# Optimization experiments

Hardware: AMD Instinct MI355X
Metric: run time of the kernel (lower is better)

The kernel has to match this reference:

```python
import jax, jax.numpy as jnp
import numpy as np

H_SIZE = 2048
NUM_K_HEADS = 16
NUM_V_HEADS = 32
DK = 128
DV = 128
KEY_DIM = NUM_K_HEADS * DK        # 2048
VALUE_DIM = NUM_V_HEADS * DV      # 4096
CONV_DIM = 2 * KEY_DIM + VALUE_DIM  # 8192
KERNEL = 4
EPS = 1e-6
B, S = 2, 2048


def setup_inputs() -> dict:
    key = jax.random.key(0)
    ks = jax.random.split(key, 8)
    w = lambda k, shape, s: jax.random.normal(k, shape, jnp.float32) * s
    return {
        "hidden_states": jax.random.normal(ks[0], (B, S, H_SIZE), jnp.float32),
        "w_qkv": w(ks[1], (H_SIZE, CONV_DIM), 0.02),
        "w_z": w(ks[2], (H_SIZE, VALUE_DIM), 0.02),
        "w_b": w(ks[3], (H_SIZE, NUM_V_HEADS), 0.02),
        "w_a": w(ks[4], (H_SIZE, NUM_V_HEADS), 0.02),
        "conv_w": w(ks[5], (CONV_DIM, KERNEL), 0.2),
        "dt_bias": jnp.ones((NUM_V_HEADS,), jnp.float32),
        "A_log": jnp.zeros((NUM_V_HEADS,), jnp.float32),
        "norm_gamma": jnp.ones((DV,), jnp.float32),
        "w_out": w(ks[6], (VALUE_DIM, H_SIZE), 0.02),
    }


def _l2norm(x, eps=1e-6):
    return x * jax.lax.rsqrt(jnp.sum(x * x, axis=-1, keepdims=True) + eps)


def _causal_conv(x, w):
    # depthwise causal conv1d; x: (B,S,C), w: (C,K)
    K = w.shape[-1]
    Sq = x.shape[1]
    xp = jnp.pad(x, ((0, 0), (K - 1, 0), (0, 0)))
    out = xp[:, 0:Sq, :] * w[None, None, :, 0]
    for j in range(1, K):  # tiny fixed kernel loop (K=4)
        out = out + xp[:, j:j + Sq, :] * w[None, None, :, j]
    return out


def _forward(hidden_states, w_qkv, w_z, w_b, w_a, conv_w, dt_bias, A_log,
             norm_gamma, w_out):
    Bq, Sq, _ = hidden_states.shape
    mixed = hidden_states @ w_qkv                       # (B,S,CONV_DIM)
    z = (hidden_states @ w_z).reshape(Bq, Sq, NUM_V_HEADS, DV)
    b = hidden_states @ w_b                             # (B,S,Hv)
    a = hidden_states @ w_a                             # (B,S,Hv)
    mixed = jax.nn.silu(_causal_conv(mixed, conv_w))
    q, k, v = jnp.split(mixed, [KEY_DIM, 2 * KEY_DIM], axis=-1)
    q = q.reshape(Bq, Sq, NUM_K_HEADS, DK)
    k = k.reshape(Bq, Sq, NUM_K_HEADS, DK)
    v = v.reshape(Bq, Sq, NUM_V_HEADS, DV)
    nrep = NUM_V_HEADS // NUM_K_HEADS
    q = jnp.repeat(q, nrep, axis=2)                     # GQA expand -> Hv heads
    k = jnp.repeat(k, nrep, axis=2)
    beta = jax.nn.sigmoid(b)                            # write gate
    g = -jnp.exp(A_log)[None, None, :] * jax.nn.softplus(a + dt_bias[None, None, :])

    # gated delta rule recurrence in float32 (matches reference)
    qf = _l2norm(q.astype(jnp.float32)) * (DK ** -0.5)
    kf = _l2norm(k.astype(jnp.float32))
    vf = v.astype(jnp.float32)
    gf = g.astype(jnp.float32)
    bf = beta.astype(jnp.float32)

    def step(state, xs):
        q_t, k_t, v_t, g_t, b_t = xs  # (B,H,dk),(B,H,dk),(B,H,dv),(B,H),(B,H)
        state = state * jnp.exp(g_t)[..., None, None]
        kv = jnp.einsum('bhk,bhkv->bhv', k_t, state)
        delta = (v_t - kv) * b_t[..., None]
        state = state + jnp.einsum('bhk,bhv->bhkv', k_t, delta)
        out = jnp.einsum('bhk,bhkv->bhv', q_t, state)
        return state, out

    mv = lambda x: jnp.moveaxis(x, 1, 0)  # (B,S,...) -> (S,B,...)
    xs = (mv(qf), mv(kf), mv(vf), mv(gf), mv(bf))
    state0 = jnp.zeros((Bq, NUM_V_HEADS, DK, DV), jnp.float32)
    _, outs = jax.lax.scan(step, state0, xs)            # (S,B,H,dv)
    o = jnp.moveaxis(outs, 0, 1)                        # (B,S,H,dv)

    # gated RMSNorm over head_v_dim: gate with silu(z), then rms-normalize
    o = o * jax.nn.silu(z.astype(jnp.float32))
    o = o * jax.lax.rsqrt(jnp.mean(o * o, axis=-1, keepdims=True) + EPS)
    o = o * norm_gamma
    o = o.reshape(Bq, Sq, VALUE_DIM).astype(hidden_states.dtype)
    return o @ w_out


def reference(hidden_states, w_qkv, w_z, w_b, w_a, conv_w, dt_bias, A_log,
              norm_gamma, w_out):
    return _forward(hidden_states, w_qkv, w_z, w_b, w_a, conv_w, dt_bias,
                    A_log, norm_gamma, w_out)
```

## Files before the change

### kernel.cpp

```cpp
#include <hip/hip_runtime.h>
#include <hip/hip_bf16.h>
#include <cstdint>


#define HSZ 2048
#define NUM_K_HEADS 16
#define NUM_V_HEADS 32
#define DKH 128
#define DVH 128
#define KEY_DIM 2048
#define VALUE_DIM 4096
#define CONV_DIM 8192
#define BB 2
#define SSEQ 2048
#define MM (BB * SSEQ)
#define CHUNK 64
#define NCHUNK (SSEQ / CHUNK)
#define DVB 16

typedef __hip_bfloat16 bf16;
typedef short short8 __attribute__((ext_vector_type(8)));
typedef float f32x4 __attribute__((ext_vector_type(4)));

__device__ __forceinline__ float bfu(ushort u) {
  union { float f; uint32_t i; } x;
  x.i = ((uint32_t)u) << 16;
  return x.f;
}
__device__ __forceinline__ ushort f2b(float f) {
  bf16 h = __float2bfloat16(f);
  return *reinterpret_cast<ushort*>(&h);
}

__device__ __forceinline__ void gload16(const void* g, const void* l) {
  __builtin_amdgcn_global_load_lds(
      (const __attribute__((address_space(1))) unsigned int*)g,
      (__attribute__((address_space(3))) unsigned int*)(const_cast<void*>(l)),
      16, 0, 0);
}

__device__ __forceinline__ int kidx(int r, int d) {
  return r * 128 + (((d >> 3) ^ (r & 7)) << 3) + (d & 7);
}
__device__ __forceinline__ int widx(int r, int d) {
  return r * 64 + (((d >> 3) ^ (r & 7)) << 3) + (d & 7);
}

__global__ __launch_bounds__(256) void cast_bf16_kernel(
    const float* __restrict__ in, ushort* __restrict__ out, int n4) {
  int i = blockIdx.x * 256 + threadIdx.x;
  if (i < n4) {
    float4 v = ((const float4*)in)[i];
    ushort4 u;
    u.x = f2b(v.x); u.y = f2b(v.y); u.z = f2b(v.z); u.w = f2b(v.w);
    ((ushort4*)out)[i] = u;
  }
}

__global__ __launch_bounds__(256) void transpose_cast(
    const float* __restrict__ W, ushort* __restrict__ WT, int K, int N) {
  __shared__ ushort tile[32][33];
  const int tx = threadIdx.x & 31, ty = threadIdx.x >> 5;
  const int n0 = blockIdx.x * 32, k0 = blockIdx.y * 32;
#pragma unroll
  for (int i = 0; i < 4; ++i)
    tile[ty + i * 8][tx] = f2b(W[(size_t)(k0 + ty + i * 8) * N + n0 + tx]);
  __syncthreads();
#pragma unroll
  for (int i = 0; i < 4; ++i)
    WT[(size_t)(n0 + ty + i * 8) * K + k0 + tx] = tile[tx][ty + i * 8];
}

__global__ __launch_bounds__(512) void gemm256(
    const ushort* __restrict__ A, const ushort* __restrict__ BT,
    ushort* __restrict__ Cv, int M, int N, int K) {
  __shared__ __align__(16) ushort smem[256 * 264];
  const int t = threadIdx.x;
  const int w = t >> 6, lane = t & 63;
  const int m0 = blockIdx.y * 256, n0 = blockIdx.x * 256;
  const int wm = (w >> 2) * 128, wn = (w & 3) * 64;
  const int fr = lane & 15, kb = lane >> 4;
  const int srow = t >> 3;
  const int scol = (t & 7) * 8;
  const int ssw = ((scol >> 3) ^ (srow & 7)) << 3;
  const int rsw = fr & 7;
  f32x4 acc[8][4] = {};
  const int nt = K / 64;

#define STAGE_TILE(tt, buf)                                                   \
  {                                                                           \
    const int k0_ = (tt)*64;                                                  \
    ushort* As_ = smem + (buf)*32768;                                         \
    ushort* Bs_ = As_ + 16384;                                                \
    _Pragma("unroll") for (int p = 0; p < 4; ++p) {                           \
      const int row_ = p * 64 + srow;                                         \
      gload16(&A[(size_t)(m0 + row_) * K + k0_ + ssw],                        \
              &As_[row_ * 64 + scol]);                                        \
    }                                                                         \
    _Pragma("unroll") for (int p = 0; p < 4; ++p) {                           \
      const int row_ = p * 64 + srow;                                         \
      gload16(&BT[(size_t)(n0 + row_) * K + k0_ + ssw],                       \
              &Bs_[row_ * 64 + scol]);                                        \
    }                                                                         \
  }

  STAGE_TILE(0, 0);
  STAGE_TILE(1, 1);

  for (int tt = 0; tt < nt; ++tt) {
    const int buf = tt & 1;
    const ushort* As = smem + buf * 32768;
    const ushort* Bs = As + 16384;
    if (tt + 1 < nt)
      asm volatile("s_waitcnt vmcnt(8)" ::: "memory");
    else
      asm volatile("s_waitcnt vmcnt(0)" ::: "memory");
    __builtin_amdgcn_sched_barrier(0);
    __builtin_amdgcn_s_barrier();
    __builtin_amdgcn_sched_barrier(0);
#pragma unroll
    for (int ks = 0; ks < 2; ++ks) {
      const int kg = ks * 4 + kb;
      const int ca = ((kg ^ rsw) << 3);
      short8 af[8], bf_[4];
#pragma unroll
      for (int mf = 0; mf < 8; ++mf)
        af[mf] = *(const short8*)&As[(wm + mf * 16 + fr) * 64 + ca];
#pragma unroll
      for (int nf = 0; nf < 4; ++nf)
        bf_[nf] = *(const short8*)&Bs[(wn + nf * 16 + fr) * 64 + ca];
#pragma unroll
      for (int mf = 0; mf < 8; ++mf)
#pragma unroll
        for (int nf = 0; nf < 4; ++nf)
          acc[mf][nf] = __builtin_amdgcn_mfma_f32_16x16x32_bf16(
              af[mf], bf_[nf], acc[mf][nf], 0, 0, 0);
    }
    __builtin_amdgcn_sched_barrier(0);
    __builtin_amdgcn_s_barrier();
    __builtin_amdgcn_sched_barrier(0);
    if (tt + 2 < nt) STAGE_TILE(tt + 2, buf);
  }
#undef STAGE_TILE

  const int crow = wm + (lane >> 4) * 4;
  const int ccol = wn + fr;
#pragma unroll
  for (int mf = 0; mf < 8; ++mf)
#pragma unroll
    for (int nf = 0; nf < 4; ++nf)
#pragma unroll
      for (int j = 0; j < 4; ++j)
        smem[(crow + mf * 16 + j) * 264 + ccol + nf * 16] = f2b(acc[mf][nf][j]);
  __syncthreads();
#pragma unroll
  for (int p = 0; p < 16; ++p) {
    const int r = p * 16 + (t >> 5), cch = (t & 31) * 8;
    *(short8*)&Cv[(size_t)(m0 + r) * N + n0 + cch] =
        *(const short8*)&smem[r * 264 + cch];
  }
}

__global__ __launch_bounds__(256, 2) void gemm128_f32(
    const ushort* __restrict__ A, const ushort* __restrict__ BT,
    float* __restrict__ C, int M, int N, int K) {
  __shared__ __align__(16) ushort smem[2 * 16384];
  const int t = threadIdx.x;
  const int w = t >> 6, lane = t & 63;
  const int m0 = blockIdx.y * 128, n0 = blockIdx.x * 128;
  const int wm = (w >> 1) * 64, wn = (w & 1) * 64;
  const int fr = lane & 15, kb = lane >> 4;
  const int srow = t >> 3;
  const int scol = (t & 7) * 8;
  const int ssw = ((scol >> 3) ^ (srow & 7)) << 3;
  const int rsw = fr & 7;
  f32x4 acc[4][4] = {};
  const int nt = K / 64;

#define STAGE128(tt, buf)                                                     \
  {                                                                           \
    const int k0_ = (tt)*64;                                                  \
    ushort* As_ = smem + (buf)*16384;                                         \
    ushort* Bs_ = As_ + 8192;                                                 \
    _Pragma("unroll") for (int p = 0; p < 4; ++p) {                           \
      const int row_ = p * 32 + srow;                                         \
      gload16(&A[(size_t)(m0 + row_) * K + k0_ + ssw],                        \
              &As_[row_ * 64 + scol]);                                        \
    }                                                                         \
    _Pragma("unroll") for (int p = 0; p < 4; ++p) {                           \
      const int row_ = p * 32 + srow;                                         \
      gload16(&BT[(size_t)(n0 + row_) * K + k0_ + ssw],                       \
              &Bs_[row_ * 64 + scol]);                                        \
    }                                                                         \
  }

  STAGE128(0, 0);
  STAGE128(1, 1);

  for (int tt = 0; tt < nt; ++tt) {
    const int buf = tt & 1;
    const ushort* As = smem + buf * 16384;
    const ushort* Bs = As + 8192;
    if (tt + 1 < nt)
      asm volatile("s_waitcnt vmcnt(8)" ::: "memory");
    else
      asm volatile("s_waitcnt vmcnt(0)" ::: "memory");
    __builtin_amdgcn_sched_barrier(0);
    __builtin_amdgcn_s_barrier();
    __builtin_amdgcn_sched_barrier(0);
#pragma unroll
    for (int ks = 0; ks < 2; ++ks) {
      const int kg = ks * 4 + kb;
      const int ca = ((kg ^ rsw) << 3);
      short8 af[4], bfr[4];
#pragma unroll
      for (int mf = 0; mf < 4; ++mf)
        af[mf] = *(const short8*)&As[(wm + mf * 16 + fr) * 64 + ca];
#pragma unroll
      for (int nf = 0; nf < 4; ++nf)
        bfr[nf] = *(const short8*)&Bs[(wn + nf * 16 + fr) * 64 + ca];
#pragma unroll
      for (int mf = 0; mf < 4; ++mf)
#pragma unroll
        for (int nf = 0; nf < 4; ++nf)
          acc[mf][nf] = __builtin_amdgcn_mfma_f32_16x16x32_bf16(
              af[mf], bfr[nf], acc[mf][nf], 0, 0, 0);
    }
    __builtin_amdgcn_sched_barrier(0);
    __builtin_amdgcn_s_barrier();
    __builtin_amdgcn_sched_barrier(0);
    if (tt + 2 < nt) STAGE128(tt + 2, buf);
  }
#undef STAGE128

  const int orow = m0 + wm + (lane >> 4) * 4;
  const int ocol = n0 + wn + fr;
#pragma unroll
  for (int mf = 0; mf < 4; ++mf)
#pragma unroll
    for (int nf = 0; nf < 4; ++nf)
#pragma unroll
      for (int j = 0; j < 4; ++j)
        C[(size_t)(orow + mf * 16 + j) * N + ocol + nf * 16] = acc[mf][nf][j];
}

__global__ __launch_bounds__(256) void ba_kernel(
    const float* __restrict__ hs, const float* __restrict__ w_b,
    const float* __restrict__ w_a, const float* __restrict__ dt_bias,
    const float* __restrict__ A_log, float* __restrict__ gbuf,
    float* __restrict__ beta) {
  const int row0 = blockIdx.x * 8;
  const int t = threadIdx.x;
  __shared__ float hsr[8][HSZ];
  __shared__ float red[2][256];
  {
    const float4* src = (const float4*)(hs + (size_t)row0 * HSZ);
    for (int i = t; i < 8 * HSZ / 4; i += 256) ((float4*)hsr)[i] = src[i];
  }
  __syncthreads();
  const int h = t & 31, p = t >> 5;
  float sb[8] = {}, sa[8] = {};
  const int kbeg = p * 256;
  for (int k = kbeg; k < kbeg + 256; ++k) {
    float wb = w_b[k * NUM_V_HEADS + h];
    float wa = w_a[k * NUM_V_HEADS + h];
#pragma unroll
    for (int r = 0; r < 8; ++r) {
      float x = hsr[r][k];
      sb[r] += x * wb;
      sa[r] += x * wa;
    }
  }
#pragma unroll
  for (int r = 0; r < 8; ++r) {
    red[0][t] = sb[r];
    red[1][t] = sa[r];
    __syncthreads();
    if (t < NUM_V_HEADS) {
      float b = 0.f, a = 0.f;
#pragma unroll
      for (int q = 0; q < 8; ++q) {
        b += red[0][t + 32 * q];
        a += red[1][t + 32 * q];
      }
      float bet = 1.f / (1.f + expf(-b));
      float x = a + dt_bias[t];
      float sp = (x > 20.f) ? x : log1pf(expf(x));
      gbuf[(size_t)(row0 + r) * NUM_V_HEADS + t] = -expf(A_log[t]) * sp;
      beta[(size_t)(row0 + r) * NUM_V_HEADS + t] = bet;
    }
    __syncthreads();
  }
}

__global__ __launch_bounds__(256) void conv_kernel(
    const ushort* __restrict__ mixed, const float* __restrict__ conv_w,
    ushort* __restrict__ qkv) {
  const int bid = blockIdx.x;
  const int slice = bid & 3;
  const int row0 = (bid >> 2) * 8;
  const int s0 = row0 & (SSEQ - 1);
  const int t = threadIdx.x;
  const int cbase = slice * 2048 + t * 8;

  float wreg[4][8];
#pragma unroll
  for (int e = 0; e < 8; ++e) {
    float4 wv = *(const float4*)&conv_w[(cbase + e) * 4];
    wreg[0][e] = wv.x;
    wreg[1][e] = wv.y;
    wreg[2][e] = wv.z;
    wreg[3][e] = wv.w;
  }

  const ushort* mp = mixed + (size_t)row0 * CONV_DIM + cbase;
  short8 win[4];
  const short8 z8 = {0, 0, 0, 0, 0, 0, 0, 0};
#pragma unroll
  for (int j = 0; j < 3; ++j)
    win[j] = (s0 - 3 + j >= 0) ? *(const short8*)&mp[(ptrdiff_t)(j - 3) * CONV_DIM]
                               : z8;

  if (slice < 2) {
    float vals[8][8];
    float ssq[8];
#pragma unroll
    for (int r = 0; r < 8; ++r) {
      win[3] = *(const short8*)&mp[(ptrdiff_t)r * CONV_DIM];
      float sq = 0.f;
#pragma unroll
      for (int e = 0; e < 8; ++e) {
        float a = bfu((ushort)win[0][e]) * wreg[0][e] +
                  bfu((ushort)win[1][e]) * wreg[1][e] +
                  bfu((ushort)win[2][e]) * wreg[2][e] +
                  bfu((ushort)win[3][e]) * wreg[3][e];
        float x = a / (1.f + expf(-a));
        vals[r][e] = x;
        sq += x * x;
      }
      ssq[r] = sq;
      win[0] = win[1];
      win[1] = win[2];
      win[2] = win[3];
    }
#pragma unroll
    for (int r = 0; r < 8; ++r) {
      float sq = ssq[r];
      sq += __shfl_xor(sq, 1, 64);
      sq += __shfl_xor(sq, 2, 64);
      sq += __shfl_xor(sq, 4, 64);
      sq += __shfl_xor(sq, 8, 64);
      float sc = rsqrtf(sq + 1e-6f);
      if (slice == 0) sc *= 0.08838834764831845f;
      short8 o;
#pragma unroll
      for (int e = 0; e < 8; ++e) o[e] = (short)f2b(vals[r][e] * sc);
      *(short8*)&qkv[(size_t)(row0 + r) * CONV_DIM + cbase] = o;
    }
  } else {
#pragma unroll
    for (int r = 0; r < 8; ++r) {
      win[3] = *(const short8*)&mp[(ptrdiff_t)r * CONV_DIM];
      short8 o;
#pragma unroll
      for (int e = 0; e < 8; ++e) {
        float a = bfu((ushort)win[0][e]) * wreg[0][e] +
                  bfu((ushort)win[1][e]) * wreg[1][e] +
                  bfu((ushort)win[2][e]) * wreg[2][e] +
                  bfu((ushort)win[3][e]) * wreg[3][e];
        o[e] = (short)f2b(a / (1.f + expf(-a)));
      }
      *(short8*)&qkv[(size_t)(row0 + r) * CONV_DIM + cbase] = o;
      win[0] = win[1];
      win[1] = win[2];
      win[2] = win[3];
    }
  }
}

__global__ __launch_bounds__(256) void chunk_T_kernel(
    const ushort* __restrict__ qkv, const float* __restrict__ gbuf,
    const float* __restrict__ beta, ushort* __restrict__ Tbuf,
    ushort* __restrict__ Wbuf) {
  const int bid = blockIdx.x;
  const int c = bid & 31;
  const int h = (bid >> 5) & 31;
  const int b = bid >> 10;
  const int hk = h >> 1;
  const int t = threadIdx.x;
  const int w = t >> 6, lane = t & 63;
  const int fr = lane & 15, fq = lane >> 4;

  __shared__ ushort Klds[64 * 128];
  __shared__ ushort Qlds[64 * 128];
  __shared__ __align__(16) float AT[64][68];
  __shared__ ushort Wlds[64 * 64];
  __shared__ float Gs[64], Bsh[64];

  const int row0 = b * SSEQ + c * CHUNK;
  const int qcol = hk * DKH;
  const int kcol = KEY_DIM + hk * DKH;

#pragma unroll
  for (int r = 0; r < 4; ++r) {
    int vi = t + 256 * r;
    int row = vi >> 4, gr = vi & 15;
    const size_t gb = (size_t)(row0 + row) * CONV_DIM;
    *(short8*)&Klds[row * 128 + ((gr ^ (row & 7)) << 3)] =
        *(const short8*)&qkv[gb + kcol + gr * 8];
    *(short8*)&Qlds[row * 128 + ((gr ^ (row & 7)) << 3)] =
        *(const short8*)&qkv[gb + qcol + gr * 8];
  }
  if (t < 64) {
    float s = gbuf[(size_t)(row0 + t) * NUM_V_HEADS + h];
#pragma unroll
    for (int off = 1; off < 64; off <<= 1) {
      float p = __shfl_up(s, off, 64);
      if (lane >= off) s += p;
    }
    Gs[t] = s;
    Bsh[t] = beta[(size_t)(row0 + t) * NUM_V_HEADS + h];
  }
  __syncthreads();

  f32x4 kkt[4] = {}, qkt[4] = {};
#pragma unroll
  for (int ks = 0; ks < 4; ++ks) {
    int d0 = ks * 32 + fq * 8;
    short8 xk = *(const short8*)&Klds[kidx(w * 16 + fr, d0)];
    short8 xq = *(const short8*)&Qlds[kidx(w * 16 + fr, d0)];
#pragma unroll
    for (int j = 0; j < 4; ++j) {
      short8 yk = *(const short8*)&Klds[kidx(j * 16 + fr, d0)];
      kkt[j] = __builtin_amdgcn_mfma_f32_16x16x32_bf16(xk, yk, kkt[j], 0, 0, 0);
      qkt[j] = __builtin_amdgcn_mfma_f32_16x16x32_bf16(xq, yk, qkt[j], 0, 0, 0);
    }
  }
#pragma unroll
  for (int j = 0; j < 4; ++j)
#pragma unroll
    for (int jj = 0; jj < 4; ++jj) {
      int i = w * 16 + fq * 4 + jj;
      int jc = j * 16 + fr;
      AT[jc][i] = (jc < i) ? Bsh[i] * __expf(Gs[i] - Gs[jc]) * kkt[j][jj] : 0.f;
      float val = (jc <= i) ? __expf(Gs[i] - Gs[jc]) * qkt[j][jj] : 0.f;
      Wlds[widx(i, jc)] = f2b(val);
    }
  __syncthreads();

  {
    ushort* Wg = Wbuf + (size_t)bid * 4096;
#pragma unroll
    for (int e = 0; e < 8; ++e)
      ((uint*)Wg)[e * 256 + t] = ((const uint*)Wlds)[e * 256 + t];
  }

  if (w == 0) {
    float u[64];
#pragma unroll
    for (int i = 0; i < 64; ++i) u[i] = (i == lane) ? 1.f : 0.f;
#pragma unroll
    for (int j = 0; j < 63; ++j) {
      float xj = u[j];
      const int i0 = (j + 1) & ~3;
#pragma unroll
      for (int ii = i0; ii < 64; ii += 4) {
        float4 a4 = *(const float4*)&AT[j][ii];
        if (ii + 0 > j) u[ii + 0] -= a4.x * xj;
        if (ii + 1 > j) u[ii + 1] -= a4.y * xj;
        if (ii + 2 > j) u[ii + 2] -= a4.z * xj;
        if (ii + 3 > j) u[ii + 3] -= a4.w * xj;
      }
    }
    ushort* Tg = Tbuf + (size_t)bid * 4096;
#pragma unroll
    for (int i = 0; i < 64; ++i) Tg[i * 64 + lane] = f2b(u[i]);
  }
}

__global__ __launch_bounds__(256, 2) void recur_chunk_kernel(
    const ushort* __restrict__ qkv, const float* __restrict__ gbuf,
    const float* __restrict__ beta, const ushort* __restrict__ Tbuf,
    const ushort* __restrict__ Wbuf, float* __restrict__ o) {
  const int bid = blockIdx.x;
  const int dvq = bid & 7;
  const int h = (bid >> 3) & 31;
  const int b = bid >> 8;
  const int hk = h >> 1;
  const int t = threadIdx.x;
  const int w = t >> 6, lane = t & 63;
  const int fr = lane & 15, fq = lane >> 4;

  __shared__ ushort Klds[64 * 128];
  __shared__ ushort Vlds[64 * DVB];
  __shared__ ushort Sth[DVB * 128];
  __shared__ ushort Stl[DVB * 128];
  __shared__ ushort Th[64 * 64];
  __shared__ ushort Wlds[64 * 64];
  __shared__ ushort Ut[DVB * 64];
  __shared__ ushort UTs[DVB * 64];
  __shared__ ushort UTo[DVB * 64];
  __shared__ float Gs[64], Bsh[64];

  float sreg[2][4] = {};

  const int qcol = hk * DKH;
  const int kcol = KEY_DIM + hk * DKH;
  const int vcol = 2 * KEY_DIM + h * DVH + dvq * DVB;
  const int ocol = h * DVH + dvq * DVB;
  const size_t tbase0 = ((size_t)(b * 32 + h) * 32) * 4096;

  for (int c = 0; c < NCHUNK; ++c) {
    const int row0 = b * SSEQ + c * CHUNK;

    short8 xq[4];
#pragma unroll
    for (int ks = 0; ks < 4; ++ks)
      xq[ks] = *(const short8*)&qkv[(size_t)(row0 + w * 16 + fr) * CONV_DIM +
                                    qcol + ks * 32 + fq * 8];
    const ushort* Tg = Tbuf + tbase0 + (size_t)c * 4096;
    const ushort* Wg = Wbuf + tbase0 + (size_t)c * 4096;
    short8 tv0 = *(const short8*)&Tg[t * 16];
    short8 tv1 = *(const short8*)&Tg[t * 16 + 8];
#pragma unroll
    for (int e = 0; e < 8; ++e)
      ((uint*)Wlds)[e * 256 + t] = ((const uint*)Wg)[e * 256 + t];
#pragma unroll
    for (int r = 0; r < 4; ++r) {
      int vi = t + 256 * r;
      int row = vi >> 4, gr = vi & 15;
      *(short8*)&Klds[row * 128 + ((gr ^ (row & 7)) << 3)] =
          *(const short8*)&qkv[(size_t)(row0 + row) * CONV_DIM + kcol + gr * 8];
    }
    if (t < 128) {
      int row = t >> 1, c0 = (t & 1) * 8;
      *(short8*)&Vlds[row * DVB + c0] =
          *(const short8*)&qkv[(size_t)(row0 + row) * CONV_DIM + vcol + c0];
    }
    if (t < 64) {
      float s = gbuf[(size_t)(row0 + t) * NUM_V_HEADS + h];
#pragma unroll
      for (int off = 1; off < 64; off <<= 1) {
        float p = __shfl_up(s, off, 64);
        if (lane >= off) s += p;
      }
      Gs[t] = s;
      Bsh[t] = beta[(size_t)(row0 + t) * NUM_V_HEADS + h];
    }
#pragma unroll
    for (int dt = 0; dt < 2; ++dt)
#pragma unroll
      for (int jj = 0; jj < 4; ++jj) {
        int d = (w * 2 + dt) * 16 + fq * 4 + jj;
        float f = sreg[dt][jj];
        ushort hi = f2b(f);
        int idx = kidx(fr, d);
        Sth[idx] = hi;
        Stl[idx] = f2b(f - bfu(hi));
      }
    {
      int r = t >> 2, d0 = (t & 3) * 16;
      *(short8*)&Th[widx(r, d0)] = tv0;
      *(short8*)&Th[widx(r, d0 + 8)] = tv1;
    }
    __syncthreads();

    f32x4 ks0 = {}, qs0 = {};
#pragma unroll
    for (int ks = 0; ks < 4; ++ks) {
      int d0 = ks * 32 + fq * 8;
      short8 xk = *(const short8*)&Klds[kidx(w * 16 + fr, d0)];
      short8 yh = *(const short8*)&Sth[kidx(fr, d0)];
      short8 yl = *(const short8*)&Stl[kidx(fr, d0)];
      ks0 = __builtin_amdgcn_mfma_f32_16x16x32_bf16(xk, yh, ks0, 0, 0, 0);
      ks0 = __builtin_amdgcn_mfma_f32_16x16x32_bf16(xk, yl, ks0, 0, 0, 0);
      qs0 = __builtin_amdgcn_mfma_f32_16x16x32_bf16(xq[ks], yh, qs0, 0, 0, 0);
      qs0 = __builtin_amdgcn_mfma_f32_16x16x32_bf16(xq[ks], yl, qs0, 0, 0, 0);
    }
    f32x4 oacc;
#pragma unroll
    for (int jj = 0; jj < 4; ++jj) {
      int i = w * 16 + fq * 4 + jj;
      float eg = __expf(Gs[i]);
      float rhs = Bsh[i] * (bfu(Vlds[i * DVB + fr]) - eg * ks0[jj]);
      Ut[widx(fr, i)] = f2b(rhs);
      oacc[jj] = qs0[jj] * eg;
    }
    __syncthreads();

    {
      f32x4 uacc = {};
#pragma unroll
      for (int ks = 0; ks < 2; ++ks) {
        int j0 = ks * 32 + fq * 8;
        short8 ta = *(const short8*)&Th[widx(w * 16 + fr, j0)];
        short8 ub = *(const short8*)&Ut[widx(fr, j0)];
        uacc = __builtin_amdgcn_mfma_f32_16x16x32_bf16(ta, ub, uacc, 0, 0, 0);
      }
#pragma unroll
      for (int jj = 0; jj < 4; ++jj) {
        int i = w * 16 + fq * 4 + jj;
        float u = uacc[jj];
        UTo[widx(fr, i)] = f2b(u);
        UTs[widx(fr, i)] = f2b(u * __expf(Gs[63] - Gs[i]));
      }
    }
    __syncthreads();

#pragma unroll
    for (int ks = 0; ks < 2; ++ks) {
      int i0 = ks * 32 + fq * 8;
      short8 xw = *(const short8*)&Wlds[widx(w * 16 + fr, i0)];
      short8 yu = *(const short8*)&UTo[widx(fr, i0)];
      oacc = __builtin_amdgcn_mfma_f32_16x16x32_bf16(xw, yu, oacc, 0, 0, 0);
    }
#pragma unroll
    for (int jj = 0; jj < 4; ++jj) {
      int tt = w * 16 + fq * 4 + jj;
      o[(size_t)(row0 + tt) * VALUE_DIM + ocol + fr] = oacc[jj];
    }
    {
      float eGC = __expf(Gs[63]);
#pragma unroll
      for (int dt = 0; dt < 2; ++dt) {
        const int dk0 = (w * 2 + dt) * 16;
        f32x4 sacc;
#pragma unroll
        for (int jj = 0; jj < 4; ++jj) sacc[jj] = sreg[dt][jj] * eGC;
        const int dkr = dk0 + fr;
#pragma unroll
        for (int ks = 0; ks < 2; ++ks) {
          short8 xk;
#pragma unroll
          for (int e = 0; e < 8; ++e)
            xk[e] = (short)Klds[kidx(ks * 32 + fq * 8 + e, dkr)];
          short8 yu = *(const short8*)&UTs[widx(fr, ks * 32 + fq * 8)];
          sacc = __builtin_amdgcn_mfma_f32_16x16x32_bf16(xk, yu, sacc, 0, 0, 0);
        }
#pragma unroll
        for (int jj = 0; jj < 4; ++jj) sreg[dt][jj] = sacc[jj];
      }
    }
    __syncthreads();
  }
}

__global__ __launch_bounds__(256) void gnorm_kernel(
    const float* __restrict__ o, const ushort* __restrict__ z,
    const float* __restrict__ gamma, ushort* __restrict__ ob) {
  const int row = blockIdx.x;
  const int t = threadIdx.x;
  const int grp = t >> 3, r = t & 7;
  const float* op = o + (size_t)row * VALUE_DIM + grp * DVH + r * 16;
  const ushort* zp = z + (size_t)row * VALUE_DIM + grp * DVH + r * 16;
  ushort* obp = ob + (size_t)row * VALUE_DIM + grp * DVH + r * 16;
  float4 ov[4];
  short8 zv[2];
#pragma unroll
  for (int q = 0; q < 4; ++q) ov[q] = *(const float4*)&op[q * 4];
  zv[0] = *(const short8*)&zp[0];
  zv[1] = *(const short8*)&zp[8];
  float vals[16];
  float ssq = 0.f;
#pragma unroll
  for (int i = 0; i < 16; ++i) {
    float zz = bfu((ushort)zv[i >> 3][i & 7]);
    float oo = ((const float*)&ov[i >> 2])[i & 3];
    float x = oo * (zz / (1.f + expf(-zz)));
    vals[i] = x;
    ssq += x * x;
  }
  ssq += __shfl_xor(ssq, 1, 64);
  ssq += __shfl_xor(ssq, 2, 64);
  ssq += __shfl_xor(ssq, 4, 64);
  float sc = rsqrtf(ssq * (1.f / 128.f) + 1e-6f);
  short8 o0, o1;
#pragma unroll
  for (int i = 0; i < 8; ++i) {
    o0[i] = (short)f2b(vals[i] * sc * gamma[r * 16 + i]);
    o1[i] = (short)f2b(vals[8 + i] * sc * gamma[r * 16 + 8 + i]);
  }
  *(short8*)&obp[0] = o0;
  *(short8*)&obp[8] = o1;
}

extern "C" void kernel_launch(void* const* d_in, const int* in_sizes, int n_in,
                              void* d_out, int out_size, void* d_ws,
                              size_t ws_size, hipStream_t stream) {
  const float* hs = (const float*)d_in[0];
  const float* w_qkv = (const float*)d_in[1];
  const float* w_z = (const float*)d_in[2];
  const float* w_b = (const float*)d_in[3];
  const float* w_a = (const float*)d_in[4];
  const float* conv_w = (const float*)d_in[5];
  const float* dt_bias = (const float*)d_in[6];
  const float* A_log = (const float*)d_in[7];
  const float* gamma = (const float*)d_in[8];
  const float* w_out = (const float*)d_in[9];
  float* out = (float*)d_out;
  char* wsb = (char*)d_ws;

  ushort* hs_b = (ushort*)wsb;
  ushort* wqkvT = hs_b + (size_t)MM * HSZ;
  ushort* wzT = wqkvT + (size_t)CONV_DIM * HSZ;
  ushort* woutT = wzT + (size_t)VALUE_DIM * HSZ;
  ushort* mixed = woutT + (size_t)HSZ * VALUE_DIM;
  ushort* qkv = mixed + (size_t)MM * CONV_DIM;
  ushort* z = qkv + (size_t)MM * CONV_DIM;
  float* gbuf = (float*)(z + (size_t)MM * VALUE_DIM);
  float* beta = gbuf + (size_t)MM * NUM_V_HEADS;
  float* o = (float*)mixed;
  ushort* ob = qkv;
  ushort* Tbuf = hs_b;
  ushort* Wbuf = wqkvT;

  cast_bf16_kernel<<<(MM * HSZ / 4 + 255) / 256, 256, 0, stream>>>(
      hs, hs_b, MM * HSZ / 4);
  transpose_cast<<<dim3(CONV_DIM / 32, HSZ / 32), 256, 0, stream>>>(
      w_qkv, wqkvT, HSZ, CONV_DIM);
  transpose_cast<<<dim3(VALUE_DIM / 32, HSZ / 32), 256, 0, stream>>>(
      w_z, wzT, HSZ, VALUE_DIM);
  transpose_cast<<<dim3(HSZ / 32, VALUE_DIM / 32), 256, 0, stream>>>(
      w_out, woutT, VALUE_DIM, HSZ);

  gemm256<<<dim3(CONV_DIM / 256, MM / 256), 512, 0, stream>>>(
      hs_b, wqkvT, mixed, MM, CONV_DIM, HSZ);
  gemm256<<<dim3(VALUE_DIM / 256, MM / 256), 512, 0, stream>>>(
      hs_b, wzT, z, MM, VALUE_DIM, HSZ);
  ba_kernel<<<MM / 8, 256, 0, stream>>>(hs, w_b, w_a, dt_bias, A_log, gbuf,
                                        beta);
  conv_kernel<<<2048, 256, 0, stream>>>(mixed, conv_w, qkv);
  chunk_T_kernel<<<2048, 256, 0, stream>>>(qkv, gbuf, beta, Tbuf, Wbuf);
  recur_chunk_kernel<<<512, 256, 0, stream>>>(qkv, gbuf, beta, Tbuf, Wbuf, o);
  gnorm_kernel<<<MM, 256, 0, stream>>>(o, z, gamma, ob);
  gemm128_f32<<<dim3(HSZ / 128, MM / 128), 256, 0, stream>>>(
      ob, woutT, out, MM, HSZ, VALUE_DIM);
}
```

Before: 695.1 us.

## Prefetch next chunk into registers in recurrence and merge qkv/z GEMM launches

The chunked delta-rule recurrence kernel now loads the next chunk's q, K, V, T, W, g and beta into registers right after the barrier. The following iteration only stores them to LDS, so global load latency overlaps the current chunk's MFMA work instead of sitting on the serial chunk path. Separately, the two input-projection GEMMs become one launch over the concatenated N dimension, routing output tiles to the mixed or z buffer. This relies on the z weight transpose being stored directly after the qkv weight transpose. The prefetch adds many live registers, which may lower occupancy or cause spills.

```diff
diff --git a/kernel.cpp b/kernel.cpp
--- a/kernel.cpp
+++ b/kernel.cpp
@@ -71,9 +71,9 @@
     WT[(size_t)(n0 + ty + i * 8) * K + k0 + tx] = tile[tx][ty + i * 8];
 }
 
-__global__ __launch_bounds__(512) void gemm256(
+__global__ __launch_bounds__(512) void gemm256_fused(
     const ushort* __restrict__ A, const ushort* __restrict__ BT,
-    ushort* __restrict__ Cv, int M, int N, int K) {
+    ushort* __restrict__ Cm, ushort* __restrict__ Cz, int M, int K) {
   __shared__ __align__(16) ushort smem[256 * 264];
   const int t = threadIdx.x;
   const int w = t >> 6, lane = t & 63;
@@ -153,10 +153,13 @@
       for (int j = 0; j < 4; ++j)
         smem[(crow + mf * 16 + j) * 264 + ccol + nf * 16] = f2b(acc[mf][nf][j]);
   __syncthreads();
+  ushort* Cout = (n0 < CONV_DIM) ? Cm : Cz;
+  const int Nout = (n0 < CONV_DIM) ? CONV_DIM : VALUE_DIM;
+  const int ncol = (n0 < CONV_DIM) ? n0 : n0 - CONV_DIM;
 #pragma unroll
   for (int p = 0; p < 16; ++p) {
     const int r = p * 16 + (t >> 5), cch = (t & 31) * 8;
-    *(short8*)&Cv[(size_t)(m0 + r) * N + n0 + cch] =
+    *(short8*)&Cout[(size_t)(m0 + r) * Nout + ncol + cch] =
         *(const short8*)&smem[r * 264 + cch];
   }
 }
@@ -510,42 +513,67 @@
   const int ocol = h * DVH + dvq * DVB;
   const size_t tbase0 = ((size_t)(b * 32 + h) * 32) * 4096;
 
-  for (int c = 0; c < NCHUNK; ++c) {
+  short8 pK[4], pT0, pT1, pV, pxq[4];
+  uint pW[8];
+  float pg = 0.f, pb = 0.f;
+
+  auto prefetch = [&](int c) {
     const int row0 = b * SSEQ + c * CHUNK;
-
-    short8 xq[4];
 #pragma unroll
     for (int ks = 0; ks < 4; ++ks)
-      xq[ks] = *(const short8*)&qkv[(size_t)(row0 + w * 16 + fr) * CONV_DIM +
-                                    qcol + ks * 32 + fq * 8];
+      pxq[ks] = *(const short8*)&qkv[(size_t)(row0 + w * 16 + fr) * CONV_DIM +
+                                     qcol + ks * 32 + fq * 8];
     const ushort* Tg = Tbuf + tbase0 + (size_t)c * 4096;
     const ushort* Wg = Wbuf + tbase0 + (size_t)c * 4096;
-    short8 tv0 = *(const short8*)&Tg[t * 16];
-    short8 tv1 = *(const short8*)&Tg[t * 16 + 8];
-#pragma unroll
-    for (int e = 0; e < 8; ++e)
-      ((uint*)Wlds)[e * 256 + t] = ((const uint*)Wg)[e * 256 + t];
+    pT0 = *(const short8*)&Tg[t * 16];
+    pT1 = *(const short8*)&Tg[t * 16 + 8];
+#pragma unroll
+    for (int e = 0; e < 8; ++e) pW[e] = ((const uint*)Wg)[e * 256 + t];
 #pragma unroll
     for (int r = 0; r < 4; ++r) {
       int vi = t + 256 * r;
       int row = vi >> 4, gr = vi & 15;
-      *(short8*)&Klds[row * 128 + ((gr ^ (row & 7)) << 3)] =
-          *(const short8*)&qkv[(size_t)(row0 + row) * CONV_DIM + kcol + gr * 8];
+      pK[r] = *(const short8*)&qkv[(size_t)(row0 + row) * CONV_DIM + kcol + gr * 8];
     }
     if (t < 128) {
       int row = t >> 1, c0 = (t & 1) * 8;
-      *(short8*)&Vlds[row * DVB + c0] =
-          *(const short8*)&qkv[(size_t)(row0 + row) * CONV_DIM + vcol + c0];
+      pV = *(const short8*)&qkv[(size_t)(row0 + row) * CONV_DIM + vcol + c0];
     }
     if (t < 64) {
-      float s = gbuf[(size_t)(row0 + t) * NUM_V_HEADS + h];
+      pg = gbuf[(size_t)(row0 + t) * NUM_V_HEADS + h];
+      pb = beta[(size_t)(row0 + t) * NUM_V_HEADS + h];
+    }
+  };
+
+  prefetch(0);
+
+  for (int c = 0; c < NCHUNK; ++c) {
+    const int row0 = b * SSEQ + c * CHUNK;
+
+    short8 xq[4];
+#pragma unroll
+    for (int ks = 0; ks < 4; ++ks) xq[ks] = pxq[ks];
+#pragma unroll
+    for (int e = 0; e < 8; ++e) ((uint*)Wlds)[e * 256 + t] = pW[e];
+#pragma unroll
+    for (int r = 0; r < 4; ++r) {
+      int vi = t + 256 * r;
+      int row = vi >> 4, gr = vi & 15;
+      *(short8*)&Klds[row * 128 + ((gr ^ (row & 7)) << 3)] = pK[r];
+    }
+    if (t < 128) {
+      int row = t >> 1, c0 = (t & 1) * 8;
+      *(short8*)&Vlds[row * DVB + c0] = pV;
+    }
+    if (t < 64) {
+      float s = pg;
 #pragma unroll
       for (int off = 1; off < 64; off <<= 1) {
         float p = __shfl_up(s, off, 64);
         if (lane >= off) s += p;
       }
       Gs[t] = s;
-      Bsh[t] = beta[(size_t)(row0 + t) * NUM_V_HEADS + h];
+      Bsh[t] = pb;
     }
 #pragma unroll
     for (int dt = 0; dt < 2; ++dt)
@@ -560,10 +588,12 @@
       }
     {
       int r = t >> 2, d0 = (t & 3) * 16;
-      *(short8*)&Th[widx(r, d0)] = tv0;
-      *(short8*)&Th[widx(r, d0 + 8)] = tv1;
+      *(short8*)&Th[widx(r, d0)] = pT0;
+      *(short8*)&Th[widx(r, d0 + 8)] = pT1;
     }
     __syncthreads();
+
+    if (c + 1 < NCHUNK) prefetch(c + 1);
 
     f32x4 ks0 = {}, qs0 = {};
 #pragma unroll
@@ -723,10 +753,8 @@
   transpose_cast<<<dim3(HSZ / 32, VALUE_DIM / 32), 256, 0, stream>>>(
       w_out, woutT, VALUE_DIM, HSZ);
 
-  gemm256<<<dim3(CONV_DIM / 256, MM / 256), 512, 0, stream>>>(
-      hs_b, wqkvT, mixed, MM, CONV_DIM, HSZ);
-  gemm256<<<dim3(VALUE_DIM / 256, MM / 256), 512, 0, stream>>>(
-      hs_b, wzT, z, MM, VALUE_DIM, HSZ);
+  gemm256_fused<<<dim3((CONV_DIM + VALUE_DIM) / 256, MM / 256), 512, 0,
+                  stream>>>(hs_b, wqkvT, mixed, z, MM, HSZ);
   ba_kernel<<<MM / 8, 256, 0, stream>>>(hs, w_b, w_a, dt_bias, A_log, gbuf,
                                         beta);
   conv_kernel<<<2048, 256, 0, stream>>>(mixed, conv_w, qkv);
```

Measured after the change: 687.4 us. No clear change (-1.1%).
